# Kernel tuning notes

Measured on AMD Instinct MI355X. Metric: run time of the kernel, lower is better.

Reference implementation:

```python
import jax, jax.numpy as jnp
import numpy as np

N = 50_000      # nodes
E = 800_000     # edges (before self-loops)
D = 128         # in_dim == out_dim
H, C = 4, 32    # GAT heads, per-head channels (out_dim // 4)
NEG_SLOPE = 0.2
LN_EPS = 1e-5


def setup_inputs() -> dict:
    key = jax.random.key(0)
    ks = jax.random.split(key, 8)
    s = 0.05
    return {
        "x": jax.random.normal(ks[0], (N, D), jnp.float32),
        "gat_W": jax.random.normal(ks[1], (D, H * C), jnp.float32) * s,
        "att_src": jax.random.normal(ks[2], (H, C), jnp.float32) * s,
        "att_dst": jax.random.normal(ks[3], (H, C), jnp.float32) * s,
        "gat_bias": jnp.zeros((H * C,), jnp.float32),
        "gcn_W": jax.random.normal(ks[4], (D, D), jnp.float32) * s,
        "gcn_bias": jnp.zeros((D,), jnp.float32),
        "gate_W": jax.random.normal(ks[5], (2 * D, 2), jnp.float32) * s,
        "gate_b": jnp.zeros((2,), jnp.float32),
        "ln_gamma": jnp.ones((D,), jnp.float32),
        "ln_beta": jnp.zeros((D,), jnp.float32),
        "edge_index": jax.random.randint(ks[6], (2, E), 0, N, jnp.int64),
    }


def reference(x, gat_W, att_src, att_dst, gat_bias, gcn_W, gcn_bias,
              gate_W, gate_b, ln_gamma, ln_beta, edge_index):
    n = x.shape[0]
    # PyG default: add self-loops for both GATConv and GCNConv
    loops = jnp.arange(n, dtype=edge_index.dtype)
    src = jnp.concatenate([edge_index[0], loops])  # message source j
    dst = jnp.concatenate([edge_index[1], loops])  # aggregation target i

    # ---------------- GATConv (heads=4, concat=True) ----------------
    h = (x @ gat_W).reshape(n, H, C)               # [N,H,C]
    a_src = jnp.einsum('nhc,hc->nh', h, att_src)   # [N,H]
    a_dst = jnp.einsum('nhc,hc->nh', h, att_dst)
    e = a_src[src] + a_dst[dst]                    # [Et,H]
    e = jnp.where(e > 0, e, NEG_SLOPE * e)         # LeakyReLU(0.2)
    e_max = jax.ops.segment_max(e, dst, num_segments=n)   # scatter-softmax, stable
    w = jnp.exp(e - e_max[dst])
    w_sum = jax.ops.segment_sum(w, dst, num_segments=n)
    alpha = w / w_sum[dst]                         # [Et,H]
    msg = alpha[:, :, None] * h[src]               # [Et,H,C]
    gat_out = jax.ops.segment_sum(msg, dst, num_segments=n).reshape(n, H * C) + gat_bias

    # ---------------- GCNConv (sym-normalized, self-loops) ----------------
    deg = jax.ops.segment_sum(jnp.ones_like(dst, dtype=x.dtype), dst, num_segments=n)
    dinv = jnp.where(deg > 0, deg ** -0.5, 0.0)
    norm = dinv[src] * dinv[dst]                   # [Et]
    g = x @ gcn_W                                  # [N,D]
    gcn_out = jax.ops.segment_sum(norm[:, None] * g[src], dst, num_segments=n) + gcn_bias

    # ---------------- gated fusion + residual + LayerNorm ----------------
    gate = jax.nn.softmax(jnp.concatenate([gat_out, gcn_out], axis=1) @ gate_W + gate_b, axis=-1)
    out = gate[:, 0:1] * gat_out + gate[:, 1:2] * gcn_out
    y = out + x
    mu = y.mean(axis=-1, keepdims=True)
    var = y.var(axis=-1, keepdims=True)
    return (y - mu) * jax.lax.rsqrt(var + LN_EPS) * ln_gamma + ln_beta
```

## Files before the change

### kernel.cpp

```cpp
#include <hip/hip_runtime.h>
#include <math.h>


typedef __attribute__((ext_vector_type(8))) short    bf16x8;
typedef __attribute__((ext_vector_type(4))) float    f32x4;
typedef __attribute__((ext_vector_type(8))) unsigned short u16x8;

__device__ __forceinline__ unsigned short f2bf(float f) {
    unsigned int u = __float_as_uint(f);
    u += 0x7fffu + ((u >> 16) & 1u);
    return (unsigned short)(u >> 16);
}
__device__ __forceinline__ float bfhi(unsigned int u) {
    return __uint_as_float(u & 0xffff0000u);
}
__device__ __forceinline__ float bflo(unsigned int u) {
    return __uint_as_float(u << 16);
}

__global__ __launch_bounds__(256) void k_prep(
    const float* __restrict__ Wg, const float* __restrict__ Wc,
    unsigned short* __restrict__ wt, int* __restrict__ counts, int n)
{
    const int t = blockIdx.x * 256 + threadIdx.x;
    const int nn = t >> 4;
    const int k0 = (t & 15) * 8;
    const float* Wsrc = (nn < 128) ? (Wg + nn) : (Wc + (nn - 128));
    u16x8 u;
    #pragma unroll
    for (int j = 0; j < 8; ++j) u[j] = f2bf(Wsrc[(size_t)(k0 + j) * 128]);
    *reinterpret_cast<u16x8*>(wt + (size_t)t * 8) = u;
    for (int i = t; i < n; i += 4096) counts[i] = 0;
}

__global__ __launch_bounds__(256) void k_combo(
    const float* __restrict__ x, const unsigned short* __restrict__ wt,
    const float* __restrict__ att_src, const float* __restrict__ att_dst,
    const int* __restrict__ dst, int* __restrict__ counts,
    unsigned short* __restrict__ pk, float* __restrict__ a_src,
    float* __restrict__ a_dst, int n, int E, int histBlocks)
{
    __shared__ unsigned short wlds[32768];
    const int t = threadIdx.x;

    if (blockIdx.x < histBlocks) {
        int i = blockIdx.x * 256 + t;
        const int stride = histBlocks * 256;
        for (; i < E; i += stride) atomicAdd(&counts[dst[i]], 1);
        return;
    }

    char* lbase = (char*)wlds;
    #pragma unroll
    for (int i = 0; i < 16; ++i) {
        const int ch = i * 256 + t;
        const int nn = ch >> 4;
        const int off = (ch & 15) * 16;
        const int byte = (nn * 256 + off) ^ ((nn & 7) << 4);
        *reinterpret_cast<u16x8*>(lbase + byte) =
            *reinterpret_cast<const u16x8*>(wt + (size_t)ch * 8);
    }
    __syncthreads();

    const int gb = blockIdx.x - histBlocks;
    const int l = t & 63;
    const int row0 = gb * 64 + (t >> 6) * 16;
    const int arow = row0 + (l & 15);
    const bool av = arow < n;
    const float* xp = x + (size_t)arow * 128 + (l >> 4) * 8;

    bf16x8 afr[4];
    #pragma unroll
    for (int ks = 0; ks < 4; ++ks) {
        float4 u0 = av ? *reinterpret_cast<const float4*>(xp + ks * 32)
                       : make_float4(0.f, 0.f, 0.f, 0.f);
        float4 u1 = av ? *reinterpret_cast<const float4*>(xp + ks * 32 + 4)
                       : make_float4(0.f, 0.f, 0.f, 0.f);
        bf16x8 a;
        a[0] = (short)f2bf(u0.x); a[1] = (short)f2bf(u0.y);
        a[2] = (short)f2bf(u0.z); a[3] = (short)f2bf(u0.w);
        a[4] = (short)f2bf(u1.x); a[5] = (short)f2bf(u1.y);
        a[6] = (short)f2bf(u1.z); a[7] = (short)f2bf(u1.w);
        afr[ks] = a;
    }

    f32x4 acc[16];
    #pragma unroll
    for (int ni = 0; ni < 16; ++ni) acc[ni] = (f32x4){0.f, 0.f, 0.f, 0.f};

    const int bco = (l & 15) * 256 + (l >> 4) * 16;
    const int bxo = (l & 7) << 4;
    #pragma unroll
    for (int ks = 0; ks < 4; ++ks) {
        #pragma unroll
        for (int ni = 0; ni < 16; ++ni) {
            const int byte = ((ni * 16) * 256 + bco + ks * 64) ^ bxo;
            const bf16x8 b = *reinterpret_cast<const bf16x8*>(lbase + byte);
            acc[ni] = __builtin_amdgcn_mfma_f32_16x16x32_bf16(afr[ks], b, acc[ni], 0, 0, 0);
        }
    }

    float ps[4][4], pd[4][4];
    #pragma unroll
    for (int h = 0; h < 4; ++h)
        #pragma unroll
        for (int q = 0; q < 4; ++q) { ps[h][q] = 0.f; pd[h][q] = 0.f; }

    #pragma unroll
    for (int ni = 0; ni < 8; ++ni) {
        const float as = att_src[ni * 16 + (l & 15)];
        const float ad = att_dst[ni * 16 + (l & 15)];
        #pragma unroll
        for (int q = 0; q < 4; ++q) {
            ps[ni >> 1][q] += acc[ni][q] * as;
            pd[ni >> 1][q] += acc[ni][q] * ad;
        }
    }
    #pragma unroll
    for (int h = 0; h < 4; ++h) {
        #pragma unroll
        for (int q = 0; q < 4; ++q) {
            float v = ps[h][q];
            v += __shfl_xor(v, 1); v += __shfl_xor(v, 2);
            v += __shfl_xor(v, 4); v += __shfl_xor(v, 8);
            ps[h][q] = v;
            float u = pd[h][q];
            u += __shfl_xor(u, 1); u += __shfl_xor(u, 2);
            u += __shfl_xor(u, 4); u += __shfl_xor(u, 8);
            pd[h][q] = u;
        }
    }
    if ((l & 15) == 0) {
        #pragma unroll
        for (int q = 0; q < 4; ++q) {
            const int row = row0 + (l >> 4) * 4 + q;
            if (row < n) {
                *reinterpret_cast<float4*>(a_src + (size_t)row * 4) =
                    make_float4(ps[0][q], ps[1][q], ps[2][q], ps[3][q]);
                *reinterpret_cast<float4*>(a_dst + (size_t)row * 4) =
                    make_float4(pd[0][q], pd[1][q], pd[2][q], pd[3][q]);
            }
        }
    }

    #pragma unroll
    for (int ni = 0; ni < 16; ++ni) {
        #pragma unroll
        for (int q = 0; q < 4; ++q) {
            const int row = row0 + (l >> 4) * 4 + q;
            if (row < n)
                pk[(size_t)row * 256 + ni * 16 + (l & 15)] = f2bf(acc[ni][q]);
        }
    }
}

__global__ __launch_bounds__(256) void k_scan1(const int* __restrict__ counts,
                                               int* __restrict__ bsum, int n)
{
    __shared__ int sh[256];
    int t = threadIdx.x;
    int i = blockIdx.x * 256 + t;
    sh[t] = (i < n) ? counts[i] : 0;
    __syncthreads();
    #pragma unroll
    for (int off = 128; off >= 1; off >>= 1) {
        if (t < off) sh[t] += sh[t + off];
        __syncthreads();
    }
    if (t == 0) bsum[blockIdx.x] = sh[0];
}

__global__ __launch_bounds__(256) void k_scan2(int* __restrict__ bsum, int nb)
{
    __shared__ int sh[256];
    int t = threadIdx.x;
    int v = (t < nb) ? bsum[t] : 0;
    sh[t] = v;
    __syncthreads();
    #pragma unroll
    for (int off = 1; off < 256; off <<= 1) {
        int u = (t >= off) ? sh[t - off] : 0;
        __syncthreads();
        sh[t] += u;
        __syncthreads();
    }
    if (t < nb) bsum[t] = sh[t] - v;
}

__global__ __launch_bounds__(256) void k_scan3(
    const int* __restrict__ counts, const int* __restrict__ bsum,
    int* __restrict__ rowptr, int* __restrict__ cursor,
    float* __restrict__ dinv, int n)
{
    __shared__ int sh[256];
    int t = threadIdx.x;
    int i = blockIdx.x * 256 + t;
    int v = (i < n) ? counts[i] : 0;
    sh[t] = v;
    __syncthreads();
    #pragma unroll
    for (int off = 1; off < 256; off <<= 1) {
        int u = (t >= off) ? sh[t - off] : 0;
        __syncthreads();
        sh[t] += u;
        __syncthreads();
    }
    if (i < n) {
        int excl = bsum[blockIdx.x] + sh[t] - v;
        rowptr[i] = excl;
        cursor[i] = excl;
        dinv[i] = rsqrtf((float)(1 + v));
        if (i == n - 1) rowptr[n] = excl + v;
    }
}

__global__ void k_scatter(const int* __restrict__ src, const int* __restrict__ dst,
                          int* __restrict__ cursor, int* __restrict__ esorted, int E)
{
    int i = blockIdx.x * blockDim.x + threadIdx.x;
    if (i < E) {
        int p = atomicAdd(&cursor[dst[i]], 1);
        esorted[p] = src[i];
    }
}

__global__ __launch_bounds__(256) void k_fused(
    const int* __restrict__ esorted, const int* __restrict__ rowptr,
    const unsigned int* __restrict__ pku,
    const float* __restrict__ a_src, const float* __restrict__ a_dst,
    const float* __restrict__ dinv, const float* __restrict__ x,
    const float* __restrict__ gat_bias, const float* __restrict__ gcn_bias,
    const float* __restrict__ gate_W, const float* __restrict__ gate_b,
    const float* __restrict__ gamma, const float* __restrict__ beta,
    float* __restrict__ out, int n)
{
    const int lane = threadIdx.x & 63;
    const int node = blockIdx.x * 4 + (threadIdx.x >> 6);
    if (node >= n) return;

    const int head = lane >> 4;
    const float adh = a_dst[node * 4 + head];
    const int beg = rowptr[node], end = rowptr[node + 1];

    float acc0 = 0.f, acc1 = 0.f, accg0 = 0.f, accg1 = 0.f, ws = 0.f;

#define EDGE_BODY(HU, GU, AV, DI)                                        \
    {                                                                    \
        float e = (AV) + adh; e = e > 0.f ? e : 0.2f * e;                \
        float w = __expf(e); ws += w;                                    \
        acc0  = fmaf(w, bflo(HU), acc0);                                 \
        acc1  = fmaf(w, bfhi(HU), acc1);                                 \
        accg0 = fmaf((DI), bflo(GU), accg0);                             \
        accg1 = fmaf((DI), bfhi(GU), accg1);                             \
    }

    int j = beg;
    for (; j + 4 <= end; j += 4) {
        const int s0 = esorted[j],     s1 = esorted[j + 1];
        const int s2 = esorted[j + 2], s3 = esorted[j + 3];
        const unsigned int h0 = pku[(size_t)s0 * 128 + lane];
        const unsigned int h1 = pku[(size_t)s1 * 128 + lane];
        const unsigned int h2 = pku[(size_t)s2 * 128 + lane];
        const unsigned int h3 = pku[(size_t)s3 * 128 + lane];
        const unsigned int g0 = pku[(size_t)s0 * 128 + 64 + lane];
        const unsigned int g1 = pku[(size_t)s1 * 128 + 64 + lane];
        const unsigned int g2 = pku[(size_t)s2 * 128 + 64 + lane];
        const unsigned int g3 = pku[(size_t)s3 * 128 + 64 + lane];
        const float a0 = a_src[s0 * 4 + head], a1 = a_src[s1 * 4 + head];
        const float a2 = a_src[s2 * 4 + head], a3 = a_src[s3 * 4 + head];
        const float d0 = dinv[s0], d1 = dinv[s1], d2 = dinv[s2], d3 = dinv[s3];
        EDGE_BODY(h0, g0, a0, d0);
        EDGE_BODY(h1, g1, a1, d1);
        EDGE_BODY(h2, g2, a2, d2);
        EDGE_BODY(h3, g3, a3, d3);
    }
    for (; j < end; ++j) {
        const int s = esorted[j];
        const unsigned int hu = pku[(size_t)s * 128 + lane];
        const unsigned int gu = pku[(size_t)s * 128 + 64 + lane];
        const float av = a_src[s * 4 + head];
        const float di = dinv[s];
        EDGE_BODY(hu, gu, av, di);
    }

    const float dvd = dinv[node];
    {
        const unsigned int hu = pku[(size_t)node * 128 + lane];
        const unsigned int gu = pku[(size_t)node * 128 + 64 + lane];
        const float av = a_src[node * 4 + head];
        EDGE_BODY(hu, gu, av, dvd);
    }
#undef EDGE_BODY

    const float2 gb2 = *reinterpret_cast<const float2*>(gat_bias + 2 * lane);
    const float2 gc2 = *reinterpret_cast<const float2*>(gcn_bias + 2 * lane);
    const float iws = 1.f / ws;
    float ga0 = acc0 * iws + gb2.x;
    float ga1 = acc1 * iws + gb2.y;
    float gc0 = accg0 * dvd + gc2.x;
    float gc1 = accg1 * dvd + gc2.y;

    const float4 gwa = *reinterpret_cast<const float4*>(gate_W + 4 * lane);
    const float4 gwb = *reinterpret_cast<const float4*>(gate_W + 256 + 4 * lane);
    float z0 = ga0 * gwa.x + ga1 * gwa.z + gc0 * gwb.x + gc1 * gwb.z;
    float z1 = ga0 * gwa.y + ga1 * gwa.w + gc0 * gwb.y + gc1 * gwb.w;
    #pragma unroll
    for (int off = 32; off >= 1; off >>= 1) {
        z0 += __shfl_xor(z0, off);
        z1 += __shfl_xor(z1, off);
    }
    z0 += gate_b[0]; z1 += gate_b[1];
    float m = fmaxf(z0, z1);
    float ez0 = __expf(z0 - m), ez1 = __expf(z1 - m);
    float inv = 1.f / (ez0 + ez1);
    float g0 = ez0 * inv, g1 = ez1 * inv;

    const size_t nbase = (size_t)node * 128;
    const float2 xv = *reinterpret_cast<const float2*>(x + nbase + 2 * lane);
    float y0 = g0 * ga0 + g1 * gc0 + xv.x;
    float y1 = g0 * ga1 + g1 * gc1 + xv.y;

    float sum = y0 + y1;
    #pragma unroll
    for (int off = 32; off >= 1; off >>= 1) sum += __shfl_xor(sum, off);
    float mu = sum * (1.f / 128.f);
    float d0v = y0 - mu, d1v = y1 - mu;
    float sq = d0v * d0v + d1v * d1v;
    #pragma unroll
    for (int off = 32; off >= 1; off >>= 1) sq += __shfl_xor(sq, off);
    float r = rsqrtf(sq * (1.f / 128.f) + 1e-5f);

    const float2 gm = *reinterpret_cast<const float2*>(gamma + 2 * lane);
    const float2 bt = *reinterpret_cast<const float2*>(beta + 2 * lane);
    float2 o;
    o.x = d0v * r * gm.x + bt.x;
    o.y = d1v * r * gm.y + bt.y;
    *reinterpret_cast<float2*>(out + nbase + 2 * lane) = o;
}

extern "C" void kernel_launch(void* const* d_in, const int* in_sizes, int n_in,
                              void* d_out, int out_size, void* d_ws, size_t ws_size,
                              hipStream_t stream)
{
    const float* x        = (const float*)d_in[0];
    const float* gat_W    = (const float*)d_in[1];
    const float* att_src  = (const float*)d_in[2];
    const float* att_dst  = (const float*)d_in[3];
    const float* gat_bias = (const float*)d_in[4];
    const float* gcn_W    = (const float*)d_in[5];
    const float* gcn_bias = (const float*)d_in[6];
    const float* gate_W   = (const float*)d_in[7];
    const float* gate_b   = (const float*)d_in[8];
    const float* ln_gamma = (const float*)d_in[9];
    const float* ln_beta  = (const float*)d_in[10];
    const int*   edge     = (const int*)d_in[11];

    const int n = in_sizes[0] / 128;
    const int E = in_sizes[11] / 2;
    const int* src = edge;
    const int* dst = edge + E;
    const int nb_chunks = (n + 255) / 256;

    char* w = (char*)d_ws;
    unsigned short* pk = (unsigned short*)w;  w += (size_t)n * 256 * 2;
    unsigned short* wt = (unsigned short*)w;  w += (size_t)256 * 128 * 2;
    float* a_src   = (float*)w;  w += (size_t)n * 4 * 4;
    float* a_dst   = (float*)w;  w += (size_t)n * 4 * 4;
    float* dinv    = (float*)w;  w += (size_t)n * 4;
    int*   counts  = (int*)w;    w += (size_t)n * 4;
    int*   bsum    = (int*)w;    w += (size_t)256 * 4;
    int*   rowptr  = (int*)w;    w += (size_t)(n + 1) * 4;
    int*   cursor  = (int*)w;    w += (size_t)n * 4;
    int*   esorted = (int*)w;    w += (size_t)E * 4;

    const int histBlocks = 512;
    const int gemmBlocks = (n + 63) / 64;

    k_prep<<<16, 256, 0, stream>>>(gat_W, gcn_W, wt, counts, n);
    k_combo<<<histBlocks + gemmBlocks, 256, 0, stream>>>(
        x, wt, att_src, att_dst, dst, counts, pk, a_src, a_dst, n, E, histBlocks);
    k_scan1<<<nb_chunks, 256, 0, stream>>>(counts, bsum, n);
    k_scan2<<<1, 256, 0, stream>>>(bsum, nb_chunks);
    k_scan3<<<nb_chunks, 256, 0, stream>>>(counts, bsum, rowptr, cursor, dinv, n);
    k_scatter<<<(E + 255) / 256, 256, 0, stream>>>(src, dst, cursor, esorted, E);
    k_fused<<<(n + 3) / 4, 256, 0, stream>>>(esorted, rowptr, (const unsigned int*)pk,
                                             a_src, a_dst, dinv, x, gat_bias, gcn_bias,
                                             gate_W, gate_b, ln_gamma, ln_beta,
                                             (float*)d_out, n);
}
```

Baseline: 268.1 us.

## Precompute edge attention weights in scatter and fold dinv into GCN features

Reorders the pipeline so the degree histogram and scans run before the GEMM. The GEMM can then pre-scale the GCN features by the source dinv and interleave the GAT and GCN bf16 pairs, so each edge needs one 8-byte load. The scatter kernel computes the per-edge exp(LeakyReLU) attention weights for all four heads and stores them in sorted order. The aggregation kernel then does no a_src or dinv gathers and no exp per edge. In exchange it adds a 16-byte-per-edge weight buffer write and read. It also no longer overlaps the histogram with the GEMM.

Measured after the change: 277.2 us. 1.03x slower.

```diff
diff --git a/kernel.cpp b/kernel.cpp
--- a/kernel.cpp
+++ b/kernel.cpp
@@ -33,22 +33,80 @@
     for (int i = t; i < n; i += 4096) counts[i] = 0;
 }
 
+__global__ void k_hist(const int* __restrict__ dst, int* __restrict__ counts, int E)
+{
+    int i = blockIdx.x * blockDim.x + threadIdx.x;
+    if (i < E) atomicAdd(&counts[dst[i]], 1);
+}
+
+__global__ __launch_bounds__(256) void k_scan1(const int* __restrict__ counts,
+                                               int* __restrict__ bsum, int n)
+{
+    __shared__ int sh[256];
+    int t = threadIdx.x;
+    int i = blockIdx.x * 256 + t;
+    sh[t] = (i < n) ? counts[i] : 0;
+    __syncthreads();
+    #pragma unroll
+    for (int off = 128; off >= 1; off >>= 1) {
+        if (t < off) sh[t] += sh[t + off];
+        __syncthreads();
+    }
+    if (t == 0) bsum[blockIdx.x] = sh[0];
+}
+
+__global__ __launch_bounds__(256) void k_scan2(int* __restrict__ bsum, int nb)
+{
+    __shared__ int sh[256];
+    int t = threadIdx.x;
+    int v = (t < nb) ? bsum[t] : 0;
+    sh[t] = v;
+    __syncthreads();
+    #pragma unroll
+    for (int off = 1; off < 256; off <<= 1) {
+        int u = (t >= off) ? sh[t - off] : 0;
+        __syncthreads();
+        sh[t] += u;
+        __syncthreads();
+    }
+    if (t < nb) bsum[t] = sh[t] - v;
+}
+
+__global__ __launch_bounds__(256) void k_scan3(
+    const int* __restrict__ counts, const int* __restrict__ bsum,
+    int* __restrict__ rowptr, int* __restrict__ cursor,
+    float* __restrict__ dinv, int n)
+{
+    __shared__ int sh[256];
+    int t = threadIdx.x;
+    int i = blockIdx.x * 256 + t;
+    int v = (i < n) ? counts[i] : 0;
+    sh[t] = v;
+    __syncthreads();
+    #pragma unroll
+    for (int off = 1; off < 256; off <<= 1) {
+        int u = (t >= off) ? sh[t - off] : 0;
+        __syncthreads();
+        sh[t] += u;
+        __syncthreads();
+    }
+    if (i < n) {
+        int excl = bsum[blockIdx.x] + sh[t] - v;
+        rowptr[i] = excl;
+        cursor[i] = excl;
+        dinv[i] = rsqrtf((float)(1 + v));
+        if (i == n - 1) rowptr[n] = excl + v;
+    }
+}
+
 __global__ __launch_bounds__(256) void k_combo(
     const float* __restrict__ x, const unsigned short* __restrict__ wt,
     const float* __restrict__ att_src, const float* __restrict__ att_dst,
-    const int* __restrict__ dst, int* __restrict__ counts,
-    unsigned short* __restrict__ pk, float* __restrict__ a_src,
-    float* __restrict__ a_dst, int n, int E, int histBlocks)
+    const float* __restrict__ dinv, unsigned short* __restrict__ pk,
+    float* __restrict__ a_src, float* __restrict__ a_dst, int n)
 {
     __shared__ unsigned short wlds[32768];
     const int t = threadIdx.x;
-
-    if (blockIdx.x < histBlocks) {
-        int i = blockIdx.x * 256 + t;
-        const int stride = histBlocks * 256;
-        for (; i < E; i += stride) atomicAdd(&counts[dst[i]], 1);
-        return;
-    }
 
     char* lbase = (char*)wlds;
     #pragma unroll
@@ -62,9 +120,8 @@
     }
     __syncthreads();
 
-    const int gb = blockIdx.x - histBlocks;
     const int l = t & 63;
-    const int row0 = gb * 64 + (t >> 6) * 16;
+    const int row0 = blockIdx.x * 64 + (t >> 6) * 16;
     const int arow = row0 + (l & 15);
     const bool av = arow < n;
     const float* xp = x + (size_t)arow * 128 + (l >> 4) * 8;
@@ -143,90 +200,52 @@
         }
     }
 
-    #pragma unroll
-    for (int ni = 0; ni < 16; ++ni) {
-        #pragma unroll
-        for (int q = 0; q < 4; ++q) {
-            const int row = row0 + (l >> 4) * 4 + q;
-            if (row < n)
-                pk[(size_t)row * 256 + ni * 16 + (l & 15)] = f2bf(acc[ni][q]);
-        }
-    }
-}
-
-__global__ __launch_bounds__(256) void k_scan1(const int* __restrict__ counts,
-                                               int* __restrict__ bsum, int n)
-{
-    __shared__ int sh[256];
-    int t = threadIdx.x;
-    int i = blockIdx.x * 256 + t;
-    sh[t] = (i < n) ? counts[i] : 0;
-    __syncthreads();
-    #pragma unroll
-    for (int off = 128; off >= 1; off >>= 1) {
-        if (t < off) sh[t] += sh[t + off];
-        __syncthreads();
-    }
-    if (t == 0) bsum[blockIdx.x] = sh[0];
-}
-
-__global__ __launch_bounds__(256) void k_scan2(int* __restrict__ bsum, int nb)
-{
-    __shared__ int sh[256];
-    int t = threadIdx.x;
-    int v = (t < nb) ? bsum[t] : 0;
-    sh[t] = v;
-    __syncthreads();
-    #pragma unroll
-    for (int off = 1; off < 256; off <<= 1) {
-        int u = (t >= off) ? sh[t - off] : 0;
-        __syncthreads();
-        sh[t] += u;
-        __syncthreads();
-    }
-    if (t < nb) bsum[t] = sh[t] - v;
-}
-
-__global__ __launch_bounds__(256) void k_scan3(
-    const int* __restrict__ counts, const int* __restrict__ bsum,
-    int* __restrict__ rowptr, int* __restrict__ cursor,
-    float* __restrict__ dinv, int n)
-{
-    __shared__ int sh[256];
-    int t = threadIdx.x;
-    int i = blockIdx.x * 256 + t;
-    int v = (i < n) ? counts[i] : 0;
-    sh[t] = v;
-    __syncthreads();
-    #pragma unroll
-    for (int off = 1; off < 256; off <<= 1) {
-        int u = (t >= off) ? sh[t - off] : 0;
-        __syncthreads();
-        sh[t] += u;
-        __syncthreads();
-    }
-    if (i < n) {
-        int excl = bsum[blockIdx.x] + sh[t] - v;
-        rowptr[i] = excl;
-        cursor[i] = excl;
-        dinv[i] = rsqrtf((float)(1 + v));
-        if (i == n - 1) rowptr[n] = excl + v;
+    const int m = l & 15;
+    const int mo = m & 1;
+    #pragma unroll
+    for (int q = 0; q < 4; ++q) {
+        const int row = row0 + (l >> 4) * 4 + q;
+        if (row >= n) continue;
+        const float dv = dinv[row];
+        unsigned short* pr = pk + (size_t)row * 256;
+        #pragma unroll
+        for (int ni = 0; ni < 8; ++ni) {
+            const int c = ni * 16 + m;
+            pr[2 * c - mo] = f2bf(acc[ni][q]);
+        }
+        #pragma unroll
+        for (int ni = 8; ni < 16; ++ni) {
+            const int cp = (ni - 8) * 16 + m;
+            pr[2 * cp + 2 - mo] = f2bf(acc[ni][q] * dv);
+        }
     }
 }
 
 __global__ void k_scatter(const int* __restrict__ src, const int* __restrict__ dst,
-                          int* __restrict__ cursor, int* __restrict__ esorted, int E)
+                          const float* __restrict__ a_src, const float* __restrict__ a_dst,
+                          int* __restrict__ cursor, int* __restrict__ esorted,
+                          float4* __restrict__ ewt, int E)
 {
     int i = blockIdx.x * blockDim.x + threadIdx.x;
-    if (i < E) {
-        int p = atomicAdd(&cursor[dst[i]], 1);
-        esorted[p] = src[i];
-    }
+    if (i >= E) return;
+    const int s = src[i], d = dst[i];
+    const float4 as = *reinterpret_cast<const float4*>(a_src + (size_t)s * 4);
+    const float4 ad = *reinterpret_cast<const float4*>(a_dst + (size_t)d * 4);
+    float4 w;
+    float e;
+    e = as.x + ad.x; e = e > 0.f ? e : 0.2f * e; w.x = __expf(e);
+    e = as.y + ad.y; e = e > 0.f ? e : 0.2f * e; w.y = __expf(e);
+    e = as.z + ad.z; e = e > 0.f ? e : 0.2f * e; w.z = __expf(e);
+    e = as.w + ad.w; e = e > 0.f ? e : 0.2f * e; w.w = __expf(e);
+    const int p = atomicAdd(&cursor[d], 1);
+    esorted[p] = s;
+    ewt[p] = w;
 }
 
 __global__ __launch_bounds__(256) void k_fused(
     const int* __restrict__ esorted, const int* __restrict__ rowptr,
-    const unsigned int* __restrict__ pku,
+    const uint2* __restrict__ pkv,
+    const float* __restrict__ ewt,
     const float* __restrict__ a_src, const float* __restrict__ a_dst,
     const float* __restrict__ dinv, const float* __restrict__ x,
     const float* __restrict__ gat_bias, const float* __restrict__ gcn_bias,
@@ -239,59 +258,53 @@
     if (node >= n) return;
 
     const int head = lane >> 4;
-    const float adh = a_dst[node * 4 + head];
     const int beg = rowptr[node], end = rowptr[node + 1];
 
     float acc0 = 0.f, acc1 = 0.f, accg0 = 0.f, accg1 = 0.f, ws = 0.f;
 
-#define EDGE_BODY(HU, GU, AV, DI)                                        \
+#define EDGE_BODY(F, W)                                                  \
     {                                                                    \
-        float e = (AV) + adh; e = e > 0.f ? e : 0.2f * e;                \
-        float w = __expf(e); ws += w;                                    \
-        acc0  = fmaf(w, bflo(HU), acc0);                                 \
-        acc1  = fmaf(w, bfhi(HU), acc1);                                 \
-        accg0 = fmaf((DI), bflo(GU), accg0);                             \
-        accg1 = fmaf((DI), bfhi(GU), accg1);                             \
+        ws += (W);                                                       \
+        acc0  = fmaf((W), bflo((F).x), acc0);                            \
+        acc1  = fmaf((W), bfhi((F).x), acc1);                            \
+        accg0 += bflo((F).y);                                            \
+        accg1 += bfhi((F).y);                                            \
     }
 
     int j = beg;
     for (; j + 4 <= end; j += 4) {
         const int s0 = esorted[j],     s1 = esorted[j + 1];
         const int s2 = esorted[j + 2], s3 = esorted[j + 3];
-        const unsigned int h0 = pku[(size_t)s0 * 128 + lane];
-        const unsigned int h1 = pku[(size_t)s1 * 128 + lane];
-        const unsigned int h2 = pku[(size_t)s2 * 128 + lane];
-        const unsigned int h3 = pku[(size_t)s3 * 128 + lane];
-        const unsigned int g0 = pku[(size_t)s0 * 128 + 64 + lane];
-        const unsigned int g1 = pku[(size_t)s1 * 128 + 64 + lane];
-        const unsigned int g2 = pku[(size_t)s2 * 128 + 64 + lane];
-        const unsigned int g3 = pku[(size_t)s3 * 128 + 64 + lane];
-        const float a0 = a_src[s0 * 4 + head], a1 = a_src[s1 * 4 + head];
-        const float a2 = a_src[s2 * 4 + head], a3 = a_src[s3 * 4 + head];
-        const float d0 = dinv[s0], d1 = dinv[s1], d2 = dinv[s2], d3 = dinv[s3];
-        EDGE_BODY(h0, g0, a0, d0);
-        EDGE_BODY(h1, g1, a1, d1);
-        EDGE_BODY(h2, g2, a2, d2);
-        EDGE_BODY(h3, g3, a3, d3);
+        const uint2 f0 = pkv[(size_t)s0 * 64 + lane];
+        const uint2 f1 = pkv[(size_t)s1 * 64 + lane];
+        const uint2 f2 = pkv[(size_t)s2 * 64 + lane];
+        const uint2 f3 = pkv[(size_t)s3 * 64 + lane];
+        const float w0 = ewt[(size_t)(j + 0) * 4 + head];
+        const float w1 = ewt[(size_t)(j + 1) * 4 + head];
+        const float w2 = ewt[(size_t)(j + 2) * 4 + head];
+        const float w3 = ewt[(size_t)(j + 3) * 4 + head];
+        EDGE_BODY(f0, w0);
+        EDGE_BODY(f1, w1);
+        EDGE_BODY(f2, w2);
+        EDGE_BODY(f3, w3);
     }
     for (; j < end; ++j) {
         const int s = esorted[j];
-        const unsigned int hu = pku[(size_t)s * 128 + lane];
-        const unsigned int gu = pku[(size_t)s * 128 + 64 + lane];
-        const float av = a_src[s * 4 + head];
-        const float di = dinv[s];
-        EDGE_BODY(hu, gu, av, di);
-    }
+        const uint2 f = pkv[(size_t)s * 64 + lane];
+        const float w = ewt[(size_t)j * 4 + head];
+        EDGE_BODY(f, w);
+    }
+
+    {
+        const uint2 f = pkv[(size_t)node * 64 + lane];
+        float e = a_src[node * 4 + head] + a_dst[node * 4 + head];
+        e = e > 0.f ? e : 0.2f * e;
+        const float w = __expf(e);
+        EDGE_BODY(f, w);
+    }
+#undef EDGE_BODY
 
     const float dvd = dinv[node];
-    {
-        const unsigned int hu = pku[(size_t)node * 128 + lane];
-        const unsigned int gu = pku[(size_t)node * 128 + 64 + lane];
-        const float av = a_src[node * 4 + head];
-        EDGE_BODY(hu, gu, av, dvd);
-    }
-#undef EDGE_BODY
-
     const float2 gb2 = *reinterpret_cast<const float2*>(gat_bias + 2 * lane);
     const float2 gc2 = *reinterpret_cast<const float2*>(gcn_bias + 2 * lane);
     const float iws = 1.f / ws;
@@ -364,6 +377,7 @@
     char* w = (char*)d_ws;
     unsigned short* pk = (unsigned short*)w;  w += (size_t)n * 256 * 2;
     unsigned short* wt = (unsigned short*)w;  w += (size_t)256 * 128 * 2;
+    float* ewt     = (float*)w;  w += (size_t)E * 4 * 4;
     float* a_src   = (float*)w;  w += (size_t)n * 4 * 4;
     float* a_dst   = (float*)w;  w += (size_t)n * 4 * 4;
     float* dinv    = (float*)w;  w += (size_t)n * 4;
@@ -373,17 +387,16 @@
     int*   cursor  = (int*)w;    w += (size_t)n * 4;
     int*   esorted = (int*)w;    w += (size_t)E * 4;
 
-    const int histBlocks = 512;
-    const int gemmBlocks = (n + 63) / 64;
-
     k_prep<<<16, 256, 0, stream>>>(gat_W, gcn_W, wt, counts, n);
-    k_combo<<<histBlocks + gemmBlocks, 256, 0, stream>>>(
-        x, wt, att_src, att_dst, dst, counts, pk, a_src, a_dst, n, E, histBlocks);
+    k_hist<<<(E + 255) / 256, 256, 0, stream>>>(dst, counts, E);
     k_scan1<<<nb_chunks, 256, 0, stream>>>(counts, bsum, n);
     k_scan2<<<1, 256, 0, stream>>>(bsum, nb_chunks);
     k_scan3<<<nb_chunks, 256, 0, stream>>>(counts, bsum, rowptr, cursor, dinv, n);
-    k_scatter<<<(E + 255) / 256, 256, 0, stream>>>(src, dst, cursor, esorted, E);
-    k_fused<<<(n + 3) / 4, 256, 0, stream>>>(esorted, rowptr, (const unsigned int*)pk,
+    k_combo<<<(n + 63) / 64, 256, 0, stream>>>(x, wt, att_src, att_dst, dinv,
+                                               pk, a_src, a_dst, n);
+    k_scatter<<<(E + 255) / 256, 256, 0, stream>>>(src, dst, a_src, a_dst, cursor,
+                                                   esorted, (float4*)ewt, E);
+    k_fused<<<(n + 3) / 4, 256, 0, stream>>>(esorted, rowptr, (const uint2*)pk, ewt,
                                              a_src, a_dst, dinv, x, gat_bias, gcn_bias,
                                              gate_W, gate_b, ln_gamma, ln_beta,
                                              (float*)d_out, n);
```
